# Kernel optimization log

Hardware: AMD Instinct MI355X
Metric: run time of the kernel (lower is better)

## Reference

```python
import jax, jax.numpy as jnp
import numpy as np

N_NODES = 100000
N_EDGES = 1600000
D_IN = 128
HID = 128
N_CLS = 10
N_GRAPHS = 128


def _gcn_conv(x, W, b, src, dst, dis, n):
    # x' = W x; out[i] = sum_{(j->i)} d_j^{-1/2} d_i^{-1/2} x'_j ; then + bias
    h = x @ W  # [N, out]
    norm = dis[src] * dis[dst]  # [E_tot]
    msg = h[src] * norm[:, None]  # gather + scale (irregular access)
    out = jax.ops.segment_sum(msg, dst, num_segments=n)  # scatter-add
    return out + b


def setup_inputs() -> dict:
    key = jax.random.key(0)
    ks = jax.random.split(key, 12)
    x = jax.random.normal(ks[0], (N_NODES, D_IN), dtype=jnp.float32)
    edge_index = jax.random.randint(ks[1], (2, N_EDGES), 0, N_NODES, dtype=jnp.int64)
    batch = jnp.sort(jax.random.randint(ks[2], (N_NODES,), 0, N_GRAPHS, dtype=jnp.int64))
    drop_u = jax.random.uniform(ks[3], (N_NODES, D_IN), dtype=jnp.float32)
    s = lambda k, sh, fan: jax.random.normal(k, sh, dtype=jnp.float32) / np.sqrt(fan)
    return {
        "x": x, "edge_index": edge_index, "batch": batch, "num_graphs": N_GRAPHS,
        "drop_u": drop_u,
        "lin1_w": s(ks[4], (D_IN, D_IN), D_IN), "lin1_b": jnp.zeros((D_IN,), jnp.float32),
        "conv1_w": s(ks[5], (D_IN, HID), D_IN), "conv1_b": jnp.zeros((HID,), jnp.float32),
        "conv2_w": s(ks[6], (HID, HID // 2), HID), "conv2_b": jnp.zeros((HID // 2,), jnp.float32),
        "lin2_w": s(ks[7], (HID // 2, N_CLS), HID // 2), "lin2_b": jnp.zeros((N_CLS,), jnp.float32),
    }


def reference(x, edge_index, batch, num_graphs, drop_u,
              lin1_w, lin1_b, conv1_w, conv1_b, conv2_w, conv2_b, lin2_w, lin2_b):
    n = x.shape[0]
    # add self loops (PyG GCNConv default)
    loop = jnp.arange(n, dtype=edge_index.dtype)
    src = jnp.concatenate([edge_index[0], loop])
    dst = jnp.concatenate([edge_index[1], loop])
    deg = jax.ops.segment_sum(jnp.ones_like(dst, dtype=x.dtype), dst, num_segments=n)
    dis = jnp.where(deg > 0, jax.lax.rsqrt(deg), 0.0)  # deg^{-1/2}

    h = x @ lin1_w + lin1_b
    h = _gcn_conv(h, conv1_w, conv1_b, src, dst, dis, n)
    # dropout p=0.5 (training mode in original): keep where u >= 0.5, scale by 2
    h = h * (drop_u >= 0.5).astype(h.dtype) * 2.0
    h = jax.nn.relu(h)
    h = _gcn_conv(h, conv2_w, conv2_b, src, dst, dis, n)
    # global mean pool over graph ids
    sums = jax.ops.segment_sum(h, batch, num_segments=num_graphs)
    cnts = jax.ops.segment_sum(jnp.ones((n,), h.dtype), batch, num_segments=num_graphs)
    pooled = sums / jnp.maximum(cnts, 1.0)[:, None]
    return pooled @ lin2_w + lin2_b
```

## Files before the change

kernel.cpp:

```cpp
#include <hip/hip_runtime.h>
#include <hip/hip_bf16.h>

#define DIN   128
#define HID2  64
#define NCLS  10
#define NGRAPH 128
#define SCAN_CHUNK 1024
#define NBLK 256
#define NBKT_MAX 512
#define CAP 6144

typedef __attribute__((ext_vector_type(8))) short bf16x8;
typedef __attribute__((ext_vector_type(4))) float f32x4;

__device__ __forceinline__ void atomAddF(float* p, float v) {
    unsafeAtomicAdd(p, v);
}

__device__ __forceinline__ unsigned short f2bf(float f) {
    unsigned int u = __float_as_uint(f);
    u += 0x7fffu + ((u >> 16) & 1u);
    return (unsigned short)(u >> 16);
}

__global__ __launch_bounds__(128) void k_w12(const float* __restrict__ lw,
                                             const float* __restrict__ lb,
                                             const float* __restrict__ cw,
                                             float* __restrict__ W12,
                                             float* __restrict__ c1preb) {
    int i = blockIdx.x, j = threadIdx.x;
    const float* arow = (i < 128) ? (lw + i * 128) : lb;
    float acc = 0.f;
#pragma unroll 8
    for (int k = 0; k < 128; ++k) acc += arow[k] * cw[k * 128 + j];
    if (i < 128) W12[i * 128 + j] = acc;
    else         c1preb[j] = acc;
}

__global__ __launch_bounds__(256) void k_bhist(const int* __restrict__ dst,
                                               int* __restrict__ bh, int E, int nbkt,
                                               float* __restrict__ zbuf, int zn) {
    __shared__ int lh[NBKT_MAX];
    if (blockIdx.x == 0)
        for (int i = threadIdx.x; i < zn; i += 256) zbuf[i] = 0.f;
    for (int i = threadIdx.x; i < nbkt; i += 256) lh[i] = 0;
    __syncthreads();
    for (int e = blockIdx.x * 256 + threadIdx.x; e < E; e += NBLK * 256)
        atomicAdd(&lh[__builtin_nontemporal_load(dst + e) >> 8], 1);
    __syncthreads();
    for (int i = threadIdx.x; i < nbkt; i += 256) bh[i * NBLK + blockIdx.x] = lh[i];
}

__global__ __launch_bounds__(256) void k_scan_part(const int* __restrict__ cnt,
                                                   int* __restrict__ part, int n) {
    int base = blockIdx.x * SCAN_CHUNK + threadIdx.x * 4;
    int s = 0;
#pragma unroll
    for (int j = 0; j < 4; ++j) { int i = base + j; if (i < n) s += cnt[i]; }
#pragma unroll
    for (int o = 32; o > 0; o >>= 1) s += __shfl_down(s, o);
    __shared__ int wsum[4];
    if ((threadIdx.x & 63) == 0) wsum[threadIdx.x >> 6] = s;
    __syncthreads();
    if (threadIdx.x == 0) part[blockIdx.x] = wsum[0] + wsum[1] + wsum[2] + wsum[3];
}
__global__ __launch_bounds__(256) void k_scan_mid(int* __restrict__ part,
                                                  int* __restrict__ total_out,
                                                  int B, int n) {
    __shared__ int sh[256];
    int t = threadIdx.x;
    int v = (t < B) ? part[t] : 0;
    sh[t] = v;
    __syncthreads();
    for (int off = 1; off < 256; off <<= 1) {
        int u = (t >= off) ? sh[t - off] : 0;
        __syncthreads();
        sh[t] += u;
        __syncthreads();
    }
    if (t < B) part[t] = sh[t] - v;
    if (t == 255) total_out[n] = sh[255];
}
__global__ __launch_bounds__(256) void k_scan_fin2(const int* cnt,
                                                   const int* __restrict__ part,
                                                   int* out, int n) {
    __shared__ int sh[256];
    int t = threadIdx.x;
    int base = blockIdx.x * SCAN_CHUNK + t * 4;
    int c[4]; int s = 0;
#pragma unroll
    for (int j = 0; j < 4; ++j) { int i = base + j; c[j] = (i < n) ? cnt[i] : 0; s += c[j]; }
    sh[t] = s;
    __syncthreads();
    for (int off = 1; off < 256; off <<= 1) {
        int u = (t >= off) ? sh[t - off] : 0;
        __syncthreads();
        sh[t] += u;
        __syncthreads();
    }
    int excl = part[blockIdx.x] + sh[t] - s;
#pragma unroll
    for (int j = 0; j < 4; ++j) {
        int i = base + j;
        if (i < n) out[i] = excl;
        excl += c[j];
    }
}

__global__ __launch_bounds__(256) void k_partition(const int* __restrict__ src,
                                                   const int* __restrict__ dst,
                                                   const int* __restrict__ bh,
                                                   int* __restrict__ pairs, int E, int nbkt) {
    __shared__ int cur[NBKT_MAX];
    for (int i = threadIdx.x; i < nbkt; i += 256) cur[i] = bh[i * NBLK + blockIdx.x];
    __syncthreads();
    for (int e = blockIdx.x * 256 + threadIdx.x; e < E; e += NBLK * 256) {
        int d = __builtin_nontemporal_load(dst + e);
        int s = __builtin_nontemporal_load(src + e);
        int pos = atomicAdd(&cur[d >> 8], 1);
        pairs[pos] = (s << 8) | (d & 255);
    }
}

__global__ __launch_bounds__(256) void k_csr_local(const int* __restrict__ pairs,
                                                   const int* __restrict__ bh,
                                                   int* __restrict__ row_start,
                                                   float* __restrict__ dis,
                                                   int* __restrict__ col,
                                                   int N) {
    __shared__ int cntL[256], scanL[256], curL[256];
    __shared__ int srcbuf[CAP];
    const int tid = threadIdx.x;
    const int lo = blockIdx.x << 8;
    const int bstart = bh[blockIdx.x * NBLK];
    const int bend = bh[(blockIdx.x + 1) * NBLK];
    const int nE = bend - bstart;

    cntL[tid] = 0;
    __syncthreads();
    for (int e = bstart + tid; e < bend; e += 256)
        atomicAdd(&cntL[pairs[e] & 255], 1);
    __syncthreads();
    const int deg = cntL[tid];
    scanL[tid] = deg;
    __syncthreads();
    for (int off = 1; off < 256; off <<= 1) {
        int u = (tid >= off) ? scanL[tid - off] : 0;
        __syncthreads();
        scanL[tid] += u;
        __syncthreads();
    }
    const int excl = scanL[tid] - deg;
    curL[tid] = excl;
    const int node = lo + tid;
    if (node < N) {
        row_start[node] = bstart + excl;
        dis[node] = rsqrtf((float)(deg + 1));
    } else if (node == N) {
        row_start[N] = bend;
    }
    __syncthreads();
    if (nE <= CAP) {
        for (int e = bstart + tid; e < bend; e += 256) {
            int p = pairs[e];
            int pos = atomicAdd(&curL[p & 255], 1);
            srcbuf[pos] = ((unsigned int)p) >> 8;
        }
        __syncthreads();
        for (int i = tid; i < nE; i += 256)
            col[bstart + i] = srcbuf[i];
    } else {
        for (int e = bstart + tid; e < bend; e += 256) {
            int p = pairs[e];
            int pos = atomicAdd(&curL[p & 255], 1);
            col[bstart + pos] = ((unsigned int)p) >> 8;
        }
    }
}

template <int NCOL>
__global__ __launch_bounds__(256) void k_gemm_mfma(const float* __restrict__ A,
                                                   const float* __restrict__ W,
                                                   const float* __restrict__ bias,
                                                   unsigned short* __restrict__ out, int M) {
    constexpr int KP = 136;
    __shared__ unsigned short As[64 * KP];
    __shared__ unsigned short Wt[NCOL * KP];

    const int tid = threadIdx.x;
    const int row0 = blockIdx.x * 64;

    for (int f = tid; f < 2048; f += 256) {
        int r = f >> 5, c4 = f & 31;
        int gr = row0 + r;
        float4 v = make_float4(0.f, 0.f, 0.f, 0.f);
        if (gr < M) v = *(const float4*)(A + (size_t)gr * 128 + c4 * 4);
        ushort4 b;
        b.x = f2bf(v.x); b.y = f2bf(v.y); b.z = f2bf(v.z); b.w = f2bf(v.w);
        *(ushort4*)(&As[r * KP + c4 * 4]) = b;
    }
    for (int f = tid; f < 32 * NCOL; f += 256) {
        int k = f / (NCOL / 4), n4 = f % (NCOL / 4);
        float4 v = *(const float4*)(W + (size_t)k * NCOL + n4 * 4);
        Wt[(n4 * 4 + 0) * KP + k] = f2bf(v.x);
        Wt[(n4 * 4 + 1) * KP + k] = f2bf(v.y);
        Wt[(n4 * 4 + 2) * KP + k] = f2bf(v.z);
        Wt[(n4 * 4 + 3) * KP + k] = f2bf(v.w);
    }
    __syncthreads();

    const int wave = tid >> 6, lane = tid & 63;
    const int quad = lane >> 4, l16 = lane & 15;
    constexpr int CT = (NCOL == 128) ? 2 : 1;
    const int col0 = wave * 16 * CT;

    f32x4 acc[4][CT];
#pragma unroll
    for (int rt = 0; rt < 4; ++rt)
#pragma unroll
        for (int ct = 0; ct < CT; ++ct) acc[rt][ct] = 0.f;

#pragma unroll
    for (int ks = 0; ks < 4; ++ks) {
        const int kbase = ks * 32 + quad * 8;
        bf16x8 bfr[CT];
#pragma unroll
        for (int ct = 0; ct < CT; ++ct)
            bfr[ct] = *(const bf16x8*)(&Wt[(col0 + ct * 16 + l16) * KP + kbase]);
#pragma unroll
        for (int rt = 0; rt < 4; ++rt) {
            bf16x8 afr = *(const bf16x8*)(&As[(rt * 16 + l16) * KP + kbase]);
#pragma unroll
            for (int ct = 0; ct < CT; ++ct)
                acc[rt][ct] = __builtin_amdgcn_mfma_f32_16x16x32_bf16(afr, bfr[ct], acc[rt][ct], 0, 0, 0);
        }
    }

#pragma unroll
    for (int rt = 0; rt < 4; ++rt)
#pragma unroll
        for (int ct = 0; ct < CT; ++ct) {
            const int c = col0 + ct * 16 + l16;
            const float bv = bias ? bias[c] : 0.f;
#pragma unroll
            for (int reg = 0; reg < 4; ++reg) {
                const int gr = row0 + rt * 16 + quad * 4 + reg;
                if (gr < M) out[(size_t)gr * NCOL + c] = f2bf(acc[rt][ct][reg] + bv);
            }
        }
}

__device__ __forceinline__ unsigned int maskbf2(unsigned int w, float ua, float ub) {
    float a = __uint_as_float(w << 16);
    float b = __uint_as_float(w & 0xffff0000u);
    a = (ua >= 0.5f) ? 2.f * fmaxf(a, 0.f) : 0.f;
    b = (ub >= 0.5f) ? 2.f * fmaxf(b, 0.f) : 0.f;
    return (unsigned int)f2bf(a) | ((unsigned int)f2bf(b) << 16);
}

__global__ __launch_bounds__(256) void k_gemm_bf16in(const unsigned short* __restrict__ A,
                                                     const float* __restrict__ W,
                                                     const float* __restrict__ du,
                                                     unsigned short* __restrict__ out, int M) {
    constexpr int NCOL = 64, KP = 136;
    __shared__ unsigned short As[64 * KP];
    __shared__ unsigned short Wt[NCOL * KP];

    const int tid = threadIdx.x;
    const int row0 = blockIdx.x * 64;

    for (int f = tid; f < 1024; f += 256) {
        int r = f >> 4, c8 = f & 15;
        int gr = row0 + r;
        uint4 b = make_uint4(0u, 0u, 0u, 0u);
        if (gr < M) {
            const uint4 v = *(const uint4*)(A + (size_t)gr * 128 + c8 * 8);
            const float4 u0 = *(const float4*)(du + (size_t)gr * 128 + c8 * 8);
            const float4 u1 = *(const float4*)(du + (size_t)gr * 128 + c8 * 8 + 4);
            b.x = maskbf2(v.x, u0.x, u0.y);
            b.y = maskbf2(v.y, u0.z, u0.w);
            b.z = maskbf2(v.z, u1.x, u1.y);
            b.w = maskbf2(v.w, u1.z, u1.w);
        }
        *(uint4*)(&As[r * KP + c8 * 8]) = b;
    }
    for (int f = tid; f < 32 * NCOL; f += 256) {
        int k = f / (NCOL / 4), n4 = f % (NCOL / 4);
        float4 v = *(const float4*)(W + (size_t)k * NCOL + n4 * 4);
        Wt[(n4 * 4 + 0) * KP + k] = f2bf(v.x);
        Wt[(n4 * 4 + 1) * KP + k] = f2bf(v.y);
        Wt[(n4 * 4 + 2) * KP + k] = f2bf(v.z);
        Wt[(n4 * 4 + 3) * KP + k] = f2bf(v.w);
    }
    __syncthreads();

    const int wave = tid >> 6, lane = tid & 63;
    const int quad = lane >> 4, l16 = lane & 15;
    const int col0 = wave * 16;

    f32x4 acc[4];
#pragma unroll
    for (int rt = 0; rt < 4; ++rt) acc[rt] = 0.f;

#pragma unroll
    for (int ks = 0; ks < 4; ++ks) {
        const int kbase = ks * 32 + quad * 8;
        bf16x8 bfr = *(const bf16x8*)(&Wt[(col0 + l16) * KP + kbase]);
#pragma unroll
        for (int rt = 0; rt < 4; ++rt) {
            bf16x8 afr = *(const bf16x8*)(&As[(rt * 16 + l16) * KP + kbase]);
            acc[rt] = __builtin_amdgcn_mfma_f32_16x16x32_bf16(afr, bfr, acc[rt], 0, 0, 0);
        }
    }

#pragma unroll
    for (int rt = 0; rt < 4; ++rt) {
        const int c = col0 + l16;
#pragma unroll
        for (int reg = 0; reg < 4; ++reg) {
            const int gr = row0 + rt * 16 + quad * 4 + reg;
            if (gr < M) out[(size_t)gr * NCOL + c] = f2bf(acc[rt][reg]);
        }
    }
}

__device__ __forceinline__ void bfacc(uint4 v, float d, float* acc) {
    acc[0] = fmaf(d, __uint_as_float(v.x << 16),        acc[0]);
    acc[1] = fmaf(d, __uint_as_float(v.x & 0xffff0000u), acc[1]);
    acc[2] = fmaf(d, __uint_as_float(v.y << 16),        acc[2]);
    acc[3] = fmaf(d, __uint_as_float(v.y & 0xffff0000u), acc[3]);
    acc[4] = fmaf(d, __uint_as_float(v.z << 16),        acc[4]);
    acc[5] = fmaf(d, __uint_as_float(v.z & 0xffff0000u), acc[5]);
    acc[6] = fmaf(d, __uint_as_float(v.w << 16),        acc[6]);
    acc[7] = fmaf(d, __uint_as_float(v.w & 0xffff0000u), acc[7]);
}

__global__ __launch_bounds__(256) void k_gather_h1(const unsigned short* __restrict__ h,
                                                   const int* __restrict__ row_start,
                                                   const int* __restrict__ col,
                                                   const float* __restrict__ dis,
                                                   const float* __restrict__ bias,
                                                   unsigned short* __restrict__ outb, int n) {
    const int node = (blockIdx.x * 256 + (int)threadIdx.x) >> 4;
    const int l = threadIdx.x & 15;
    if (node >= n) return;
    const int coff = l * 8;

    const float dn = dis[node];
    float acc[8];
    {
        uint4 v = *(const uint4*)(h + (size_t)node * 128 + coff);
#pragma unroll
        for (int q = 0; q < 8; ++q) acc[q] = 0.f;
        bfacc(v, dn, acc);
    }

    const int beg = row_start[node], end = row_start[node + 1];
    int j = beg;
    for (; j + 3 < end; j += 4) {
        const int s0 = col[j], s1 = col[j + 1], s2 = col[j + 2], s3 = col[j + 3];
        const float d0 = dis[s0], d1 = dis[s1], d2 = dis[s2], d3 = dis[s3];
        const uint4 v0 = *(const uint4*)(h + (size_t)s0 * 128 + coff);
        const uint4 v1 = *(const uint4*)(h + (size_t)s1 * 128 + coff);
        const uint4 v2 = *(const uint4*)(h + (size_t)s2 * 128 + coff);
        const uint4 v3 = *(const uint4*)(h + (size_t)s3 * 128 + coff);
        bfacc(v0, d0, acc);
        bfacc(v1, d1, acc);
        bfacc(v2, d2, acc);
        bfacc(v3, d3, acc);
    }
    for (; j < end; ++j) {
        const int s0 = col[j];
        const float d0 = dis[s0];
        const uint4 v0 = *(const uint4*)(h + (size_t)s0 * 128 + coff);
        bfacc(v0, d0, acc);
    }

    const float4 b0 = *(const float4*)(bias + coff);
    const float4 b1 = *(const float4*)(bias + coff + 4);
    const float r0 = fmaf(dn, acc[0], b0.x), r1 = fmaf(dn, acc[1], b0.y);
    const float r2 = fmaf(dn, acc[2], b0.z), r3 = fmaf(dn, acc[3], b0.w);
    const float r4 = fmaf(dn, acc[4], b1.x), r5 = fmaf(dn, acc[5], b1.y);
    const float r6 = fmaf(dn, acc[6], b1.z), r7 = fmaf(dn, acc[7], b1.w);
    uint4 o;
    o.x = (unsigned int)f2bf(r0) | ((unsigned int)f2bf(r1) << 16);
    o.y = (unsigned int)f2bf(r2) | ((unsigned int)f2bf(r3) << 16);
    o.z = (unsigned int)f2bf(r4) | ((unsigned int)f2bf(r5) << 16);
    o.w = (unsigned int)f2bf(r6) | ((unsigned int)f2bf(r7) << 16);
    *(uint4*)(outb + (size_t)node * 128 + coff) = o;
}

__global__ __launch_bounds__(256) void k_gather_pool(const unsigned short* __restrict__ h,
                                                     const int* __restrict__ row_start,
                                                     const int* __restrict__ col,
                                                     const float* __restrict__ dis,
                                                     const float* __restrict__ bias,
                                                     const int* __restrict__ batch,
                                                     float* __restrict__ partial,
                                                     int* __restrict__ bgid,
                                                     int* __restrict__ bvcnt,
                                                     float* __restrict__ sums,
                                                     float* __restrict__ cnt, int n) {
    __shared__ float bsum[4][64];
    __shared__ int sh_gfirst, sh_uni;
    const int tid = threadIdx.x;
    const int node = (blockIdx.x * 256 + tid) >> 3;
    const int l = tid & 7;
    const int coff = l * 8;
    const bool valid = node < n;
    const int node0 = blockIdx.x * 32;

    if (tid == 0) { sh_gfirst = batch[node0]; sh_uni = 1; }
    __syncthreads();
    const int gfirst = sh_gfirst;

    float r[8];
    int g = gfirst;
    if (valid) {
        const float dn = dis[node];
        g = batch[node];
        float acc[8];
        {
            uint4 v = *(const uint4*)(h + (size_t)node * 64 + coff);
#pragma unroll
            for (int q = 0; q < 8; ++q) acc[q] = 0.f;
            bfacc(v, dn, acc);
        }
        const int beg = row_start[node], end = row_start[node + 1];
        int j = beg;
        for (; j + 3 < end; j += 4) {
            const int s0 = col[j], s1 = col[j + 1], s2 = col[j + 2], s3 = col[j + 3];
            const float d0 = dis[s0], d1 = dis[s1], d2 = dis[s2], d3 = dis[s3];
            const uint4 v0 = *(const uint4*)(h + (size_t)s0 * 64 + coff);
            const uint4 v1 = *(const uint4*)(h + (size_t)s1 * 64 + coff);
            const uint4 v2 = *(const uint4*)(h + (size_t)s2 * 64 + coff);
            const uint4 v3 = *(const uint4*)(h + (size_t)s3 * 64 + coff);
            bfacc(v0, d0, acc);
            bfacc(v1, d1, acc);
            bfacc(v2, d2, acc);
            bfacc(v3, d3, acc);
        }
        for (; j < end; ++j) {
            const int s0 = col[j];
            const float d0 = dis[s0];
            const uint4 v0 = *(const uint4*)(h + (size_t)s0 * 64 + coff);
            bfacc(v0, d0, acc);
        }
        const float4 b0 = *(const float4*)(bias + coff);
        const float4 b1 = *(const float4*)(bias + coff + 4);
        r[0] = fmaf(dn, acc[0], b0.x); r[1] = fmaf(dn, acc[1], b0.y);
        r[2] = fmaf(dn, acc[2], b0.z); r[3] = fmaf(dn, acc[3], b0.w);
        r[4] = fmaf(dn, acc[4], b1.x); r[5] = fmaf(dn, acc[5], b1.y);
        r[6] = fmaf(dn, acc[6], b1.z); r[7] = fmaf(dn, acc[7], b1.w);
    } else {
#pragma unroll
        for (int q = 0; q < 8; ++q) r[q] = 0.f;
    }

    if (valid && g != gfirst) atomicAnd(&sh_uni, 0);
    __syncthreads();

    if (sh_uni) {
#pragma unroll
        for (int q = 0; q < 8; ++q) {
            r[q] += __shfl_xor(r[q], 8);
            r[q] += __shfl_xor(r[q], 16);
            r[q] += __shfl_xor(r[q], 32);
        }
        const int wave = tid >> 6, lane = tid & 63;
        if (lane < 8) {
#pragma unroll
            for (int q = 0; q < 8; ++q) bsum[wave][lane * 8 + q] = r[q];
        }
        __syncthreads();
        if (tid < 64)
            partial[(size_t)blockIdx.x * 64 + tid] =
                bsum[0][tid] + bsum[1][tid] + bsum[2][tid] + bsum[3][tid];
        if (tid == 0) {
            bgid[blockIdx.x] = gfirst;
            bvcnt[blockIdx.x] = min(n - node0, 32);
        }
    } else {
        if (tid == 0) bgid[blockIdx.x] = -1;
        const int g0 = __shfl(g, 0);
        const bool wuni = __all(valid && (g == g0));
        if (wuni) {
#pragma unroll
            for (int q = 0; q < 8; ++q) {
                r[q] += __shfl_xor(r[q], 8);
                r[q] += __shfl_xor(r[q], 16);
                r[q] += __shfl_xor(r[q], 32);
            }
            const int lane = tid & 63;
            if (lane < 8) {
#pragma unroll
                for (int q = 0; q < 8; ++q) atomAddF(&sums[g0 * 64 + lane * 8 + q], r[q]);
                if (lane == 0) atomAddF(&cnt[g0], 8.0f);
            }
        } else if (valid) {
#pragma unroll
            for (int q = 0; q < 8; ++q) atomAddF(&sums[g * 64 + coff + q], r[q]);
            if (l == 0) atomAddF(&cnt[g], 1.0f);
        }
    }
}

__global__ __launch_bounds__(256) void k_pool2(const float* __restrict__ partial,
                                               const int* __restrict__ bgid,
                                               const int* __restrict__ bvcnt,
                                               float* __restrict__ sums,
                                               float* __restrict__ cnt, int nb) {
    const int grp = (blockIdx.x * 256 + (int)threadIdx.x) >> 6;
    const int f = threadIdx.x & 63;
    const int ngroups = gridDim.x * 4;
    const int per = (nb + ngroups - 1) / ngroups;
    const int start = grp * per, end = min(nb, start + per);
    if (start >= end) return;
    int cg = -1;
    float acc = 0.f;
    int vc = 0;
    for (int b = start; b < end; ++b) {
        const int g = bgid[b];
        if (g != cg) {
            if (cg >= 0) {
                atomAddF(&sums[cg * 64 + f], acc);
                if (f == 0) atomAddF(&cnt[cg], (float)vc);
            }
            acc = 0.f; vc = 0; cg = g;
        }
        if (g >= 0) {
            acc += partial[(size_t)b * 64 + f];
            vc += bvcnt[b];
        }
    }
    if (cg >= 0) {
        atomAddF(&sums[cg * 64 + f], acc);
        if (f == 0) atomAddF(&cnt[cg], (float)vc);
    }
}

__global__ __launch_bounds__(64) void k_final(const float* __restrict__ sums,
                                              const float* __restrict__ cnt,
                                              const float* __restrict__ w,
                                              const float* __restrict__ b,
                                              float* __restrict__ out) {
    int g = blockIdx.x, f = threadIdx.x;
    float c = fmaxf(cnt[g], 1.0f);
    float p = sums[g * 64 + f] / c;
#pragma unroll
    for (int cls = 0; cls < NCLS; ++cls) {
        float v = p * w[f * 10 + cls];
#pragma unroll
        for (int o = 32; o > 0; o >>= 1) v += __shfl_down(v, o);
        if (f == 0) out[g * 10 + cls] = v + b[cls];
    }
}

extern "C" void kernel_launch(void* const* d_in, const int* in_sizes, int n_in,
                              void* d_out, int out_size, void* d_ws, size_t ws_size,
                              hipStream_t stream) {
    const float* x       = (const float*)d_in[0];
    const int*   ei      = (const int*)d_in[1];
    const int*   batch   = (const int*)d_in[2];
    const float* drop_u  = (const float*)d_in[4];
    const float* lin1_w  = (const float*)d_in[5];
    const float* lin1_b  = (const float*)d_in[6];
    const float* conv1_w = (const float*)d_in[7];
    const float* conv1_b = (const float*)d_in[8];
    const float* conv2_w = (const float*)d_in[9];
    const float* conv2_b = (const float*)d_in[10];
    const float* lin2_w  = (const float*)d_in[11];
    const float* lin2_b  = (const float*)d_in[12];
    float* out = (float*)d_out;

    const int N = in_sizes[0] / DIN;
    const int E = in_sizes[1] / 2;
    const int* src = ei;
    const int* dst = ei + E;

    const int nbkt = (N + 255) >> 8;
    const int M = nbkt * NBLK;
    const int nbGP = (int)(((size_t)N * 8 + 255) / 256);

    float* ws    = (float*)d_ws;
    float* out1  = ws;
    unsigned short* h1b = (unsigned short*)(ws + (size_t)N * 128);
    float* dis   = ws + (size_t)N * 128 + (size_t)N * 64;
    float* W12   = dis + N;
    float* c1pb  = W12 + 16384;
    float* sums  = c1pb + 128;
    float* cntp  = sums + NGRAPH * 64;
    int*   row_start = (int*)(cntp + NGRAPH);
    int*   part  = row_start + N + 2;
    int*   bh    = part + 256;
    int*   col   = bh + NBKT_MAX * NBLK + 2;
    int*   pairs = col + E;
    float* partial = (float*)(pairs + E);
    int*   bgid  = (int*)(partial + (size_t)nbGP * 64);
    int*   bvcnt = bgid + nbGP;
    unsigned short* h1agg = (unsigned short*)out1;
    unsigned short* h2b = h1b;

    k_w12<<<129, 128, 0, stream>>>(lin1_w, lin1_b, conv1_w, W12, c1pb);

    k_bhist<<<NBLK, 256, 0, stream>>>(dst, bh, E, nbkt, sums, NGRAPH * 64 + NGRAPH);
    const int scanB = (M + SCAN_CHUNK - 1) / SCAN_CHUNK;
    k_scan_part<<<scanB, 256, 0, stream>>>(bh, part, M);
    k_scan_mid<<<1, 256, 0, stream>>>(part, bh, scanB, M);
    k_scan_fin2<<<scanB, 256, 0, stream>>>(bh, part, bh, M);
    k_partition<<<NBLK, 256, 0, stream>>>(src, dst, bh, pairs, E, nbkt);
    k_csr_local<<<nbkt, 256, 0, stream>>>(pairs, bh, row_start, dis, col, N);

    const int gemmGrid = (N + 63) / 64;
    k_gemm_mfma<128><<<gemmGrid, 256, 0, stream>>>(x, W12, c1pb, h1b, N);

    k_gather_h1<<<((size_t)N * 16 + 255) / 256, 256, 0, stream>>>(h1b, row_start, col, dis, conv1_b, h1agg, N);

    k_gemm_bf16in<<<gemmGrid, 256, 0, stream>>>(h1agg, conv2_w, drop_u, h2b, N);

    k_gather_pool<<<nbGP, 256, 0, stream>>>(h2b, row_start, col, dis, conv2_b, batch,
                                            partial, bgid, bvcnt, sums, cntp, N);
    k_pool2<<<16, 256, 0, stream>>>(partial, bgid, bvcnt, sums, cntp, nbGP);

    k_final<<<NGRAPH, 64, 0, stream>>>(sums, cntp, lin2_w, lin2_b, out);
}
```

Measured before the change: 386.6 us.

## Fuse conv1 gather with dropout/relu and conv2 GEMM into one kernel

Merges the first GCN aggregation, the dropout+ReLU masking and the second MFMA GEMM into a single kernel. Each 16-node block keeps its aggregated rows in LDS and multiplies them by conv2 weights, which are pre-converted to bf16 once by an extra block in the weight-prep kernel. This removes the write and re-read of the 100k×128 bf16 intermediate and one launch. In exchange, every 16-node block reloads and transposes the full 64×128 weight tile into LDS, and the MFMA work per block is small.

Result: no change. 379.6 us (-1.8%).

```diff
diff --git a/kernel.cpp b/kernel.cpp
--- a/kernel.cpp
+++ b/kernel.cpp
@@ -26,9 +26,15 @@
 __global__ __launch_bounds__(128) void k_w12(const float* __restrict__ lw,
                                              const float* __restrict__ lb,
                                              const float* __restrict__ cw,
+                                             const float* __restrict__ cw2,
                                              float* __restrict__ W12,
-                                             float* __restrict__ c1preb) {
+                                             float* __restrict__ c1preb,
+                                             unsigned short* __restrict__ w2b) {
     int i = blockIdx.x, j = threadIdx.x;
+    if (i == 129) {
+        for (int f = j; f < 8192; f += 128) w2b[f] = f2bf(cw2[f]);
+        return;
+    }
     const float* arow = (i < 128) ? (lw + i * 128) : lb;
     float acc = 0.f;
 #pragma unroll 8
@@ -250,80 +256,6 @@
         }
 }
 
-__device__ __forceinline__ unsigned int maskbf2(unsigned int w, float ua, float ub) {
-    float a = __uint_as_float(w << 16);
-    float b = __uint_as_float(w & 0xffff0000u);
-    a = (ua >= 0.5f) ? 2.f * fmaxf(a, 0.f) : 0.f;
-    b = (ub >= 0.5f) ? 2.f * fmaxf(b, 0.f) : 0.f;
-    return (unsigned int)f2bf(a) | ((unsigned int)f2bf(b) << 16);
-}
-
-__global__ __launch_bounds__(256) void k_gemm_bf16in(const unsigned short* __restrict__ A,
-                                                     const float* __restrict__ W,
-                                                     const float* __restrict__ du,
-                                                     unsigned short* __restrict__ out, int M) {
-    constexpr int NCOL = 64, KP = 136;
-    __shared__ unsigned short As[64 * KP];
-    __shared__ unsigned short Wt[NCOL * KP];
-
-    const int tid = threadIdx.x;
-    const int row0 = blockIdx.x * 64;
-
-    for (int f = tid; f < 1024; f += 256) {
-        int r = f >> 4, c8 = f & 15;
-        int gr = row0 + r;
-        uint4 b = make_uint4(0u, 0u, 0u, 0u);
-        if (gr < M) {
-            const uint4 v = *(const uint4*)(A + (size_t)gr * 128 + c8 * 8);
-            const float4 u0 = *(const float4*)(du + (size_t)gr * 128 + c8 * 8);
-            const float4 u1 = *(const float4*)(du + (size_t)gr * 128 + c8 * 8 + 4);
-            b.x = maskbf2(v.x, u0.x, u0.y);
-            b.y = maskbf2(v.y, u0.z, u0.w);
-            b.z = maskbf2(v.z, u1.x, u1.y);
-            b.w = maskbf2(v.w, u1.z, u1.w);
-        }
-        *(uint4*)(&As[r * KP + c8 * 8]) = b;
-    }
-    for (int f = tid; f < 32 * NCOL; f += 256) {
-        int k = f / (NCOL / 4), n4 = f % (NCOL / 4);
-        float4 v = *(const float4*)(W + (size_t)k * NCOL + n4 * 4);
-        Wt[(n4 * 4 + 0) * KP + k] = f2bf(v.x);
-        Wt[(n4 * 4 + 1) * KP + k] = f2bf(v.y);
-        Wt[(n4 * 4 + 2) * KP + k] = f2bf(v.z);
-        Wt[(n4 * 4 + 3) * KP + k] = f2bf(v.w);
-    }
-    __syncthreads();
-
-    const int wave = tid >> 6, lane = tid & 63;
-    const int quad = lane >> 4, l16 = lane & 15;
-    const int col0 = wave * 16;
-
-    f32x4 acc[4];
-#pragma unroll
-    for (int rt = 0; rt < 4; ++rt) acc[rt] = 0.f;
-
-#pragma unroll
-    for (int ks = 0; ks < 4; ++ks) {
-        const int kbase = ks * 32 + quad * 8;
-        bf16x8 bfr = *(const bf16x8*)(&Wt[(col0 + l16) * KP + kbase]);
-#pragma unroll
-        for (int rt = 0; rt < 4; ++rt) {
-            bf16x8 afr = *(const bf16x8*)(&As[(rt * 16 + l16) * KP + kbase]);
-            acc[rt] = __builtin_amdgcn_mfma_f32_16x16x32_bf16(afr, bfr, acc[rt], 0, 0, 0);
-        }
-    }
-
-#pragma unroll
-    for (int rt = 0; rt < 4; ++rt) {
-        const int c = col0 + l16;
-#pragma unroll
-        for (int reg = 0; reg < 4; ++reg) {
-            const int gr = row0 + rt * 16 + quad * 4 + reg;
-            if (gr < M) out[(size_t)gr * NCOL + c] = f2bf(acc[rt][reg]);
-        }
-    }
-}
-
 __device__ __forceinline__ void bfacc(uint4 v, float d, float* acc) {
     acc[0] = fmaf(d, __uint_as_float(v.x << 16),        acc[0]);
     acc[1] = fmaf(d, __uint_as_float(v.x & 0xffff0000u), acc[1]);
@@ -335,59 +267,102 @@
     acc[7] = fmaf(d, __uint_as_float(v.w & 0xffff0000u), acc[7]);
 }
 
-__global__ __launch_bounds__(256) void k_gather_h1(const unsigned short* __restrict__ h,
-                                                   const int* __restrict__ row_start,
-                                                   const int* __restrict__ col,
-                                                   const float* __restrict__ dis,
-                                                   const float* __restrict__ bias,
-                                                   unsigned short* __restrict__ outb, int n) {
-    const int node = (blockIdx.x * 256 + (int)threadIdx.x) >> 4;
-    const int l = threadIdx.x & 15;
-    if (node >= n) return;
+__global__ __launch_bounds__(256) void k_gather_gemm2(const unsigned short* __restrict__ h,
+                                                      const int* __restrict__ row_start,
+                                                      const int* __restrict__ col,
+                                                      const float* __restrict__ dis,
+                                                      const float* __restrict__ bias,
+                                                      const float* __restrict__ du,
+                                                      const unsigned short* __restrict__ w2b,
+                                                      unsigned short* __restrict__ h2b,
+                                                      int n) {
+    constexpr int KP = 136;
+    __shared__ unsigned short As[16 * KP];
+    __shared__ unsigned short Wt[64 * KP];
+    const int tid = threadIdx.x;
+    const int node0 = blockIdx.x * 16;
+    const int node = node0 + (tid >> 4);
+    const int l = tid & 15;
     const int coff = l * 8;
 
-    const float dn = dis[node];
-    float acc[8];
-    {
-        uint4 v = *(const uint4*)(h + (size_t)node * 128 + coff);
-#pragma unroll
-        for (int q = 0; q < 8; ++q) acc[q] = 0.f;
-        bfacc(v, dn, acc);
-    }
-
-    const int beg = row_start[node], end = row_start[node + 1];
-    int j = beg;
-    for (; j + 3 < end; j += 4) {
-        const int s0 = col[j], s1 = col[j + 1], s2 = col[j + 2], s3 = col[j + 3];
-        const float d0 = dis[s0], d1 = dis[s1], d2 = dis[s2], d3 = dis[s3];
-        const uint4 v0 = *(const uint4*)(h + (size_t)s0 * 128 + coff);
-        const uint4 v1 = *(const uint4*)(h + (size_t)s1 * 128 + coff);
-        const uint4 v2 = *(const uint4*)(h + (size_t)s2 * 128 + coff);
-        const uint4 v3 = *(const uint4*)(h + (size_t)s3 * 128 + coff);
-        bfacc(v0, d0, acc);
-        bfacc(v1, d1, acc);
-        bfacc(v2, d2, acc);
-        bfacc(v3, d3, acc);
-    }
-    for (; j < end; ++j) {
-        const int s0 = col[j];
-        const float d0 = dis[s0];
-        const uint4 v0 = *(const uint4*)(h + (size_t)s0 * 128 + coff);
-        bfacc(v0, d0, acc);
-    }
-
-    const float4 b0 = *(const float4*)(bias + coff);
-    const float4 b1 = *(const float4*)(bias + coff + 4);
-    const float r0 = fmaf(dn, acc[0], b0.x), r1 = fmaf(dn, acc[1], b0.y);
-    const float r2 = fmaf(dn, acc[2], b0.z), r3 = fmaf(dn, acc[3], b0.w);
-    const float r4 = fmaf(dn, acc[4], b1.x), r5 = fmaf(dn, acc[5], b1.y);
-    const float r6 = fmaf(dn, acc[6], b1.z), r7 = fmaf(dn, acc[7], b1.w);
-    uint4 o;
-    o.x = (unsigned int)f2bf(r0) | ((unsigned int)f2bf(r1) << 16);
-    o.y = (unsigned int)f2bf(r2) | ((unsigned int)f2bf(r3) << 16);
-    o.z = (unsigned int)f2bf(r4) | ((unsigned int)f2bf(r5) << 16);
-    o.w = (unsigned int)f2bf(r6) | ((unsigned int)f2bf(r7) << 16);
-    *(uint4*)(outb + (size_t)node * 128 + coff) = o;
+    for (int f = tid; f < 8192; f += 256) {
+        int k = f >> 6, c = f & 63;
+        Wt[c * KP + k] = w2b[f];
+    }
+
+    float r[8];
+    if (node < n) {
+        const float dn = dis[node];
+        float acc[8];
+        {
+            uint4 v = *(const uint4*)(h + (size_t)node * 128 + coff);
+#pragma unroll
+            for (int q = 0; q < 8; ++q) acc[q] = 0.f;
+            bfacc(v, dn, acc);
+        }
+        const int beg = row_start[node], end = row_start[node + 1];
+        int j = beg;
+        for (; j + 3 < end; j += 4) {
+            const int s0 = col[j], s1 = col[j + 1], s2 = col[j + 2], s3 = col[j + 3];
+            const float d0 = dis[s0], d1 = dis[s1], d2 = dis[s2], d3 = dis[s3];
+            const uint4 v0 = *(const uint4*)(h + (size_t)s0 * 128 + coff);
+            const uint4 v1 = *(const uint4*)(h + (size_t)s1 * 128 + coff);
+            const uint4 v2 = *(const uint4*)(h + (size_t)s2 * 128 + coff);
+            const uint4 v3 = *(const uint4*)(h + (size_t)s3 * 128 + coff);
+            bfacc(v0, d0, acc);
+            bfacc(v1, d1, acc);
+            bfacc(v2, d2, acc);
+            bfacc(v3, d3, acc);
+        }
+        for (; j < end; ++j) {
+            const int s0 = col[j];
+            const float d0 = dis[s0];
+            const uint4 v0 = *(const uint4*)(h + (size_t)s0 * 128 + coff);
+            bfacc(v0, d0, acc);
+        }
+        const float4 b0 = *(const float4*)(bias + coff);
+        const float4 b1 = *(const float4*)(bias + coff + 4);
+        r[0] = fmaf(dn, acc[0], b0.x); r[1] = fmaf(dn, acc[1], b0.y);
+        r[2] = fmaf(dn, acc[2], b0.z); r[3] = fmaf(dn, acc[3], b0.w);
+        r[4] = fmaf(dn, acc[4], b1.x); r[5] = fmaf(dn, acc[5], b1.y);
+        r[6] = fmaf(dn, acc[6], b1.z); r[7] = fmaf(dn, acc[7], b1.w);
+        const float4 u0 = *(const float4*)(du + (size_t)node * 128 + coff);
+        const float4 u1 = *(const float4*)(du + (size_t)node * 128 + coff + 4);
+        r[0] = (u0.x >= 0.5f) ? 2.f * fmaxf(r[0], 0.f) : 0.f;
+        r[1] = (u0.y >= 0.5f) ? 2.f * fmaxf(r[1], 0.f) : 0.f;
+        r[2] = (u0.z >= 0.5f) ? 2.f * fmaxf(r[2], 0.f) : 0.f;
+        r[3] = (u0.w >= 0.5f) ? 2.f * fmaxf(r[3], 0.f) : 0.f;
+        r[4] = (u1.x >= 0.5f) ? 2.f * fmaxf(r[4], 0.f) : 0.f;
+        r[5] = (u1.y >= 0.5f) ? 2.f * fmaxf(r[5], 0.f) : 0.f;
+        r[6] = (u1.z >= 0.5f) ? 2.f * fmaxf(r[6], 0.f) : 0.f;
+        r[7] = (u1.w >= 0.5f) ? 2.f * fmaxf(r[7], 0.f) : 0.f;
+    } else {
+#pragma unroll
+        for (int q = 0; q < 8; ++q) r[q] = 0.f;
+    }
+    ushort4 o0, o1;
+    o0.x = f2bf(r[0]); o0.y = f2bf(r[1]); o0.z = f2bf(r[2]); o0.w = f2bf(r[3]);
+    o1.x = f2bf(r[4]); o1.y = f2bf(r[5]); o1.z = f2bf(r[6]); o1.w = f2bf(r[7]);
+    *(ushort4*)(&As[(tid >> 4) * KP + coff]) = o0;
+    *(ushort4*)(&As[(tid >> 4) * KP + coff + 4]) = o1;
+    __syncthreads();
+
+    const int wave = tid >> 6, lane = tid & 63;
+    const int quad = lane >> 4, l16 = lane & 15;
+    const int c0 = wave * 16;
+    f32x4 a2 = 0.f;
+#pragma unroll
+    for (int ks = 0; ks < 4; ++ks) {
+        const int kbase = ks * 32 + quad * 8;
+        bf16x8 afr = *(const bf16x8*)(&As[l16 * KP + kbase]);
+        bf16x8 bfr = *(const bf16x8*)(&Wt[(c0 + l16) * KP + kbase]);
+        a2 = __builtin_amdgcn_mfma_f32_16x16x32_bf16(afr, bfr, a2, 0, 0, 0);
+    }
+#pragma unroll
+    for (int reg = 0; reg < 4; ++reg) {
+        const int gr = node0 + quad * 4 + reg;
+        if (gr < n) h2b[(size_t)gr * 64 + c0 + l16] = f2bf(a2[reg]);
+    }
 }
 
 __global__ __launch_bounds__(256) void k_gather_pool(const unsigned short* __restrict__ h,
@@ -598,10 +573,10 @@
     float* partial = (float*)(pairs + E);
     int*   bgid  = (int*)(partial + (size_t)nbGP * 64);
     int*   bvcnt = bgid + nbGP;
-    unsigned short* h1agg = (unsigned short*)out1;
-    unsigned short* h2b = h1b;
-
-    k_w12<<<129, 128, 0, stream>>>(lin1_w, lin1_b, conv1_w, W12, c1pb);
+    unsigned short* h2b = (unsigned short*)out1;
+    unsigned short* w2b = (unsigned short*)(out1 + (size_t)N * 64);
+
+    k_w12<<<130, 128, 0, stream>>>(lin1_w, lin1_b, conv1_w, conv2_w, W12, c1pb, w2b);
 
     k_bhist<<<NBLK, 256, 0, stream>>>(dst, bh, E, nbkt, sums, NGRAPH * 64 + NGRAPH);
     const int scanB = (M + SCAN_CHUNK - 1) / SCAN_CHUNK;
@@ -614,9 +589,8 @@
     const int gemmGrid = (N + 63) / 64;
     k_gemm_mfma<128><<<gemmGrid, 256, 0, stream>>>(x, W12, c1pb, h1b, N);
 
-    k_gather_h1<<<((size_t)N * 16 + 255) / 256, 256, 0, stream>>>(h1b, row_start, col, dis, conv1_b, h1agg, N);
-
-    k_gemm_bf16in<<<gemmGrid, 256, 0, stream>>>(h1agg, conv2_w, drop_u, h2b, N);
+    k_gather_gemm2<<<(N + 15) / 16, 256, 0, stream>>>(h1b, row_start, col, dis, conv1_b,
+                                                      drop_u, w2b, h2b, N);
 
     k_gather_pool<<<nbGP, 256, 0, stream>>>(h2b, row_start, col, dis, conv2_b, batch,
                                             partial, bgid, bvcnt, sums, cntp, N);
```
